# Kernel optimization log

Measured on AMD Instinct MI355X. Metric: run time of the kernel, lower is better.

The kernel has to match this reference:

```python
import jax, jax.numpy as jnp
import numpy as np

K = 8192   # codebook_size
D = 256    # latent_dim
COMMITMENT_COST = 0.25


def setup_inputs() -> dict:
    key = jax.random.key(0)
    kx, kw = jax.random.split(key)
    x = jax.random.normal(kx, (8, 4096, D), dtype=jnp.float32)
    # nn.init.uniform_(weight, -1/K, 1/K)
    weight = jax.random.uniform(kw, (K, D), dtype=jnp.float32,
                                minval=-1.0 / K, maxval=1.0 / K)
    return {"x": x, "weight": weight}


def reference(x, weight):
    sg = jax.lax.stop_gradient
    orig_shape = x.shape
    x_flat = x.reshape(-1, D)                      # [N, D]
    # squared euclidean distances; argmin identical to cdist argmin
    x_sq = jnp.sum(x_flat * x_flat, axis=-1, keepdims=True)      # [N, 1]
    w_sq = jnp.sum(weight * weight, axis=-1)                     # [K]
    dist2 = x_sq - 2.0 * (x_flat @ weight.T) + w_sq              # [N, K]
    indices = jnp.argmin(dist2, axis=1)                          # [N]
    quantized = jnp.take(weight, indices, axis=0).reshape(orig_shape)
    # eval / non-EMA branch of the torch module
    commitment_loss = jnp.mean((x - sg(quantized)) ** 2) * COMMITMENT_COST
    codebook_loss = jnp.mean((quantized - sg(x)) ** 2)
    total = commitment_loss + codebook_loss
    # straight-through estimator
    quantized_st = x + sg(quantized - x)
    indices_out = indices.reshape(orig_shape[:-1])
    return quantized_st, indices_out, commitment_loss, codebook_loss, total
```

## Files before the change

### kernel.cpp

```cpp
#include <hip/hip_runtime.h>

#define K_CB   8192
#define D_DIM  256
#define N_ROWS 32768
#define Q_ELEMS (N_ROWS * D_DIM)

#define M_FLAG 1.3e-4f
#define M_CAND 1.3e-4f
#define CAP    16

typedef __bf16 bf16x8 __attribute__((ext_vector_type(8)));
typedef float  f32x16 __attribute__((ext_vector_type(16)));

#define ASYNC_COPY16(gp, lp)                                              \
    __builtin_amdgcn_global_load_lds(                                     \
        (const __attribute__((address_space(1))) unsigned int*)(gp),      \
        (__attribute__((address_space(3))) unsigned int*)(lp), 16, 0, 0)


__device__ inline ushort f2bf(float f) {
    unsigned u = __float_as_uint(f);
    unsigned r = u + 0x7FFFu + ((u >> 16) & 1u);
    return (ushort)(r >> 16);
}

__device__ inline uint4 pack8(float4 a, float4 b) {
    uint4 o;
    o.x = (unsigned)f2bf(a.x) | ((unsigned)f2bf(a.y) << 16);
    o.y = (unsigned)f2bf(a.z) | ((unsigned)f2bf(a.w) << 16);
    o.z = (unsigned)f2bf(b.x) | ((unsigned)f2bf(b.y) << 16);
    o.w = (unsigned)f2bf(b.z) | ((unsigned)f2bf(b.w) << 16);
    return o;
}

__global__ __launch_bounds__(256) void wsq_wbf_kernel(const float* __restrict__ w,
                                                      float* __restrict__ wsq,
                                                      ushort* __restrict__ wbf) {
    __shared__ __align__(16) ushort tile[64 * 256];
    const int t = threadIdx.x;
    const int kb = blockIdx.x;
    const int wv = t >> 6, lane = t & 63;

    const float4* wb = reinterpret_cast<const float4*>(w) + (size_t)kb * 4096;
    #pragma unroll
    for (int i = 0; i < 16; ++i) {
        int j = i * 256 + t;
        float4 v = wb[j];
        int c = j >> 6, d4 = j & 63;
        uint2 o;
        o.x = (unsigned)f2bf(-2.0f * v.x) | ((unsigned)f2bf(-2.0f * v.y) << 16);
        o.y = (unsigned)f2bf(-2.0f * v.z) | ((unsigned)f2bf(-2.0f * v.w) << 16);
        *reinterpret_cast<uint2*>((char*)tile + (size_t)(d4 >> 1) * 1024 + c * 16 + (d4 & 1) * 8) = o;
    }

    for (int c = wv; c < 64; c += 4) {
        float4 v = reinterpret_cast<const float4*>(w)[(size_t)(kb * 64 + c) * 64 + lane];
        double sq = (double)v.x * v.x + (double)v.y * v.y + (double)v.z * v.z + (double)v.w * v.w;
        #pragma unroll
        for (int off = 32; off > 0; off >>= 1) sq += __shfl_down(sq, off, 64);
        if (lane == 0) wsq[kb * 64 + c] = (float)sq;
    }

    __syncthreads();
    const uint4* src = reinterpret_cast<const uint4*>(tile);
    uint4* dst = reinterpret_cast<uint4*>((char*)wbf + (size_t)kb * 32768);
    #pragma unroll
    for (int j = 0; j < 8; ++j) dst[j * 256 + t] = src[j * 256 + t];
}

__global__ __launch_bounds__(512, 2) void pass1_kernel(
        const float* __restrict__ x, const ushort* __restrict__ wbf,
        const float* __restrict__ wsq, float* __restrict__ idx_out,
        float* __restrict__ rowmin, int* __restrict__ flags,
        unsigned* __restrict__ flag_count, int* __restrict__ hard_flags,
        unsigned* __restrict__ hard_count, int* __restrict__ candcnt,
        int* __restrict__ cands) {
    __shared__ __align__(16) char smem[66560];
    ushort* wt = reinterpret_cast<ushort*>(smem);

    const int t = threadIdx.x;
    const int lane = t & 63, ln31 = lane & 31, h = lane >> 5;
    const int wv = t >> 6;
    const int rs = wv >> 1, cs = wv & 1;
    const int colL = cs * 32 + ln31;
    const int r0 = blockIdx.x * 128;

    {
        const char* g = (const char*)wbf + (size_t)wv * 4096 + (size_t)lane * 16;
        char* l = (char*)wt + wv * 4096;
        #pragma unroll
        for (int i = 0; i < 4; ++i) ASYNC_COPY16(g + i * 1024, l + i * 1024);
    }

    const int arow = r0 + rs * 32 + ln31;
    const float4* xr = reinterpret_cast<const float4*>(x) + (size_t)arow * 64;
    bf16x8 afr[16];
    #pragma unroll
    for (int kk = 0; kk < 16; ++kk)
        afr[kk] = __builtin_bit_cast(bf16x8, pack8(xr[kk * 4 + h * 2], xr[kk * 4 + h * 2 + 1]));

    float b1[16], b2[16];
    #pragma unroll
    for (int r = 0; r < 16; ++r) { b1[r] = 3.4e38f; b2[r] = 3.4e38f; }

    __syncthreads();

    int cur = 0;
    for (int it = 0; it < 128; ++it) {
        float wsk = wsq[it * 64 + colL];
        {
            const char* g = (const char*)wbf + (size_t)((it + 1) & 127) * 32768
                          + (size_t)wv * 4096 + (size_t)lane * 16;
            char* l = (char*)wt + (cur ^ 1) * 32768 + wv * 4096;
            #pragma unroll
            for (int i = 0; i < 4; ++i) ASYNC_COPY16(g + i * 1024, l + i * 1024);
        }

        const ushort* bt = wt + cur * 16384;
        f32x16 acc = {0,0,0,0,0,0,0,0,0,0,0,0,0,0,0,0};
        #pragma unroll
        for (int kk = 0; kk < 16; ++kk) {
            bf16x8 bf = *reinterpret_cast<const bf16x8*>(&bt[(size_t)(kk * 2 + h) * 512 + colL * 8]);
            acc = __builtin_amdgcn_mfma_f32_32x32x16_bf16(afr[kk], bf, acc, 0, 0, 0);
        }

        const int kb = it * 64 + colL;
        #pragma unroll
        for (int r = 0; r < 16; ++r) {
            float s0 = acc[r] + wsk;
            float p0 = __uint_as_float((__float_as_uint(s0) & 0xFFFFE000u) | (unsigned)kb);
            b2[r] = __builtin_amdgcn_fmed3f(p0, b1[r], b2[r]);
            b1[r] = fminf(p0, b1[r]);
        }

        __syncthreads();
        cur ^= 1;
    }

    float* sb1 = reinterpret_cast<float*>(smem);
    float* sb2 = sb1 + 128 * 65;
    #pragma unroll
    for (int r = 0; r < 16; ++r) {
        int rl = rs * 32 + (r & 3) + 8 * (r >> 2) + 4 * h;
        sb1[rl * 65 + colL] = b1[r];
        sb2[rl * 65 + colL] = b2[r];
    }
    __syncthreads();
    if (t < 128) {
        float B1 = 3.4e38f, B2 = 3.4e38f;
        for (int c = 0; c < 64; ++c) {
            float a1 = sb1[t * 65 + c], a2 = sb2[t * 65 + c];
            float nb2 = fminf(fmaxf(B1, a1), fminf(B2, a2));
            B1 = fminf(B1, a1);
            B2 = nb2;
        }
        int row = r0 + t;
        idx_out[row] = (float)(__float_as_uint(B1) & 0x1FFFu);
        rowmin[row]  = B1;
        int nc = 0;
        if (B2 - B1 <= M_FLAG) {
            unsigned pos = atomicAdd(flag_count, 1u);
            if (pos < N_ROWS) flags[pos] = row;
            float T = B1 + M_CAND;
            bool hard = false;
            for (int c = 0; c < 64; ++c) {
                float a1 = sb1[t * 65 + c];
                if (a1 <= T) {
                    if (nc < CAP) cands[row * CAP + nc] = (int)(__float_as_uint(a1) & 0x1FFFu);
                    ++nc;
                }
                if (sb2[t * 65 + c] <= T) hard = true;
            }
            if (nc > CAP) hard = true;
            if (hard) {
                nc = 0;
                unsigned hp = atomicAdd(hard_count, 1u);
                if (hp < N_ROWS) hard_flags[hp] = row;
            }
        }
        candcnt[row] = nc;
    }
}

__global__ __launch_bounds__(256, 2) void fixup_kernel(
        const float* __restrict__ x, const ushort* __restrict__ wbf,
        const float* __restrict__ wsq, const float* __restrict__ rowmin,
        const int* __restrict__ hard_flags, const unsigned* __restrict__ hard_count,
        int* __restrict__ candcnt, int* __restrict__ cands) {
    __shared__ __align__(16) ushort wt[64 * 256];
    __shared__ int   sh_rows[64];
    __shared__ float sh_thr[64];

    const int t = threadIdx.x;
    const int lane = t & 63, ln31 = lane & 31, h = lane >> 5;
    const int wv = t >> 6, rs = wv & 1, cs = wv >> 1;
    const int colL = cs * 32 + ln31;

    unsigned cu = hard_count[0];
    int cnt = cu > N_ROWS ? N_ROWS : (int)cu;
    int nunits = ((cnt + 63) >> 6) * 8;

    for (int u = blockIdx.x; u < nunits; u += 512) {
        int ksp  = u & 7;
        int base = (u >> 3) * 64;
        int nrows = cnt - base; if (nrows > 64) nrows = 64;

        __syncthreads();
        if (t < 64) {
            int valid = (t < nrows);
            int gr = hard_flags[base + (valid ? t : 0)];
            sh_rows[t] = gr;
            sh_thr[t]  = valid ? rowmin[gr] + M_CAND : -3.4e38f;
        }
        __syncthreads();

        int arow = sh_rows[rs * 32 + ln31];
        const float4* xr = reinterpret_cast<const float4*>(x) + (size_t)arow * 64;
        bf16x8 afr[16];
        #pragma unroll
        for (int kk = 0; kk < 16; ++kk)
            afr[kk] = __builtin_bit_cast(bf16x8, pack8(xr[kk * 4 + h * 2], xr[kk * 4 + h * 2 + 1]));
        float thr_r[16];
        int   rl_r[16];
        #pragma unroll
        for (int r = 0; r < 16; ++r) {
            rl_r[r]  = rs * 32 + (r & 3) + 8 * (r >> 2) + 4 * h;
            thr_r[r] = sh_thr[rl_r[r]];
        }

        for (int tb = 0; tb < 16; ++tb) {
            int blk = ksp * 16 + tb;
            __syncthreads();
            {
                const char* g = (const char*)wbf + (size_t)blk * 32768
                              + (size_t)wv * 8192 + (size_t)lane * 16;
                char* l = (char*)wt + wv * 8192;
                #pragma unroll
                for (int i = 0; i < 8; ++i) ASYNC_COPY16(g + i * 1024, l + i * 1024);
            }
            __syncthreads();

            int kcol = blk * 64 + colL;
            float wsk = wsq[kcol];
            f32x16 acc = {0,0,0,0,0,0,0,0,0,0,0,0,0,0,0,0};
            #pragma unroll
            for (int kk = 0; kk < 16; ++kk) {
                bf16x8 bf = *reinterpret_cast<const bf16x8*>(&wt[(size_t)(kk * 2 + h) * 512 + colL * 8]);
                acc = __builtin_amdgcn_mfma_f32_32x32x16_bf16(afr[kk], bf, acc, 0, 0, 0);
            }
            #pragma unroll
            for (int r = 0; r < 16; ++r) {
                float s0 = acc[r] + wsk;
                if (s0 <= thr_r[r]) {
                    int grow = sh_rows[rl_r[r]];
                    int pos = atomicAdd(&candcnt[grow], 1);
                    if (pos < CAP) cands[grow * CAP + pos] = kcol;
                }
            }
        }
    }
}

__global__ __launch_bounds__(256) void rescore_kernel(
        const float* __restrict__ x, const float* __restrict__ w,
        const float* __restrict__ wsq,
        const int* __restrict__ flags, const unsigned* __restrict__ flag_count,
        const int* __restrict__ candcnt, const int* __restrict__ cands,
        float* __restrict__ idx_out) {
    int wid  = (blockIdx.x * 256 + threadIdx.x) >> 6;
    int lane = threadIdx.x & 63;
    unsigned cu = flag_count[0];
    int cnt = (cu > N_ROWS) ? N_ROWS : (int)cu;

    for (int fi = wid; fi < cnt; fi += 1024) {
        int row = flags[fi];
        float4 xv = reinterpret_cast<const float4*>(x)[(size_t)row * 64 + lane];
        double xs = (double)xv.x * xv.x + (double)xv.y * xv.y
                  + (double)xv.z * xv.z + (double)xv.w * xv.w;
        #pragma unroll
        for (int off = 1; off < 64; off <<= 1) xs += __shfl_xor(xs, off, 64);
        float Xs = (float)xs;
        int nc = candcnt[row]; if (nc > CAP) nc = CAP;
        float bq = 3.4e38f; int bk = -1;
        for (int c = 0; c < nc; ++c) {
            int k = cands[row * CAP + c];
            float4 wv = reinterpret_cast<const float4*>(w)[(size_t)k * 64 + lane];
            double d = (double)xv.x * wv.x + (double)xv.y * wv.y
                     + (double)xv.z * wv.z + (double)xv.w * wv.w;
            #pragma unroll
            for (int off = 1; off < 64; off <<= 1) d += __shfl_xor(d, off, 64);
            float XW = (float)d;
            float t3 = fmaf(-2.0f, XW, Xs);
            float qv = t3 + wsq[k];
            if (qv < bq || (qv == bq && k < bk) || bk < 0) { bq = qv; bk = k; }
        }
        if (lane == 0 && bk >= 0) idx_out[row] = (float)bk;
    }
}

__global__ __launch_bounds__(256) void gather_loss_kernel(
        const float* __restrict__ x, const float* __restrict__ w,
        const float* __restrict__ idx_f, float* __restrict__ out_q,
        float* __restrict__ accum) {
    const int nf4 = Q_ELEMS / 4;
    float lsum = 0.0f;
    for (int e = blockIdx.x * blockDim.x + threadIdx.x; e < nf4;
         e += gridDim.x * blockDim.x) {
        int row = e >> 6, d4 = e & 63;
        int k = (int)idx_f[row];
        float4 xv = reinterpret_cast<const float4*>(x)[e];
        float4 qv = reinterpret_cast<const float4*>(w)[(size_t)k * 64 + d4];
        float4 ov;
        ov.x = xv.x + (qv.x - xv.x);
        ov.y = xv.y + (qv.y - xv.y);
        ov.z = xv.z + (qv.z - xv.z);
        ov.w = xv.w + (qv.w - xv.w);
        reinterpret_cast<float4*>(out_q)[e] = ov;
        float dx = xv.x - qv.x, dy = xv.y - qv.y, dz = xv.z - qv.z, dw = xv.w - qv.w;
        lsum += dx * dx + dy * dy + dz * dz + dw * dw;
    }
    #pragma unroll
    for (int off = 32; off > 0; off >>= 1) lsum += __shfl_down(lsum, off, 64);
    __shared__ float ssum[4];
    if ((threadIdx.x & 63) == 0) ssum[threadIdx.x >> 6] = lsum;
    __syncthreads();
    if (threadIdx.x == 0)
        atomicAdd(accum, ssum[0] + ssum[1] + ssum[2] + ssum[3]);
}

__global__ void finalize_kernel(const float* __restrict__ accum,
                                float* __restrict__ out_tail) {
    float mse = accum[0] / (float)Q_ELEMS;
    float commit = 0.25f * mse;
    out_tail[0] = commit;
    out_tail[1] = mse;
    out_tail[2] = commit + mse;
}

extern "C" void kernel_launch(void* const* d_in, const int* in_sizes, int n_in,
                              void* d_out, int out_size, void* d_ws, size_t ws_size,
                              hipStream_t stream) {
    const float* x = (const float*)d_in[0];
    const float* w = (const float*)d_in[1];
    float* out = (float*)d_out;

    char* ws = (char*)d_ws;
    float*    Wsq        = (float*)ws;
    float*    Rmin       = (float*)(ws + 163840);
    float*    accum      = (float*)(ws + 294912);
    unsigned* flag_count = (unsigned*)(ws + 294916);
    unsigned* hard_count = (unsigned*)(ws + 294920);
    int*      flags      = (int*)(ws + 294924);
    int*      hard_flags = (int*)(ws + 425996);
    int*      candcnt    = (int*)(ws + 557068);
    int*      cands      = (int*)(ws + 688140);
    ushort*   Wbf        = (ushort*)(ws + 2785296);

    hipMemsetAsync(ws + 294912, 0, 12, stream);
    wsq_wbf_kernel<<<K_CB / 64, 256, 0, stream>>>(w, Wsq, Wbf);
    pass1_kernel<<<N_ROWS / 128, 512, 0, stream>>>(x, Wbf, Wsq, out + Q_ELEMS,
                                                   Rmin, flags, flag_count,
                                                   hard_flags, hard_count,
                                                   candcnt, cands);
    fixup_kernel<<<512, 256, 0, stream>>>(x, Wbf, Wsq, Rmin, hard_flags, hard_count,
                                          candcnt, cands);
    rescore_kernel<<<256, 256, 0, stream>>>(x, w, Wsq, flags, flag_count,
                                            candcnt, cands, out + Q_ELEMS);
    gather_loss_kernel<<<8192, 256, 0, stream>>>(x, w, out + Q_ELEMS, out, accum);
    finalize_kernel<<<1, 1, 0, stream>>>(accum, out + Q_ELEMS + N_ROWS);
}
```

Baseline: 408.5 us.

## Deepen codebook LDS pipeline to four stages with single barrier per iteration

Replaces the double-buffered codebook tile pipeline in pass1 with a 4-slot ring that prefetches three tiles ahead. The per-tile squared norms are now staged into LDS alongside the weights. Each iteration uses explicit vmcnt waits plus a single barrier instead of a trailing __syncthreads, and raises wave priority around the MFMA loop. The aim is to hide global-load latency and cut barrier stalls, but LDS grows to about 135KB per block, which likely drops occupancy from two blocks per CU to one despite launch_bounds(512,2).

```diff
diff --git a/kernel.cpp b/kernel.cpp
--- a/kernel.cpp
+++ b/kernel.cpp
@@ -75,8 +75,7 @@
         unsigned* __restrict__ flag_count, int* __restrict__ hard_flags,
         unsigned* __restrict__ hard_count, int* __restrict__ candcnt,
         int* __restrict__ cands) {
-    __shared__ __align__(16) char smem[66560];
-    ushort* wt = reinterpret_cast<ushort*>(smem);
+    __shared__ __align__(16) char smem[135168];
 
     const int t = threadIdx.x;
     const int lane = t & 63, ln31 = lane & 31, h = lane >> 5;
@@ -85,11 +84,16 @@
     const int colL = cs * 32 + ln31;
     const int r0 = blockIdx.x * 128;
 
-    {
-        const char* g = (const char*)wbf + (size_t)wv * 4096 + (size_t)lane * 16;
-        char* l = (char*)wt + wv * 4096;
+    const char* gWb = (const char*)wbf + (size_t)wv * 4096 + (size_t)lane * 16;
+    const char* gQb = (const char*)wsq + (size_t)lane * 16;
+
+    #pragma unroll
+    for (int p = 0; p < 3; ++p) {
+        const char* g = gWb + (size_t)p * 32768;
+        char* l = smem + p * 33792 + wv * 4096;
         #pragma unroll
         for (int i = 0; i < 4; ++i) ASYNC_COPY16(g + i * 1024, l + i * 1024);
+        if (wv == 0) ASYNC_COPY16(gQb + p * 256, smem + p * 33792 + 32768);
     }
 
     const int arow = r0 + rs * 32 + ln31;
@@ -103,26 +107,33 @@
     #pragma unroll
     for (int r = 0; r < 16; ++r) { b1[r] = 3.4e38f; b2[r] = 3.4e38f; }
 
-    __syncthreads();
-
-    int cur = 0;
     for (int it = 0; it < 128; ++it) {
-        float wsk = wsq[it * 64 + colL];
+        if (wv == 0) { asm volatile("s_waitcnt vmcnt(10)" ::: "memory"); }
+        else         { asm volatile("s_waitcnt vmcnt(8)"  ::: "memory"); }
+        __builtin_amdgcn_s_barrier();
+
         {
-            const char* g = (const char*)wbf + (size_t)((it + 1) & 127) * 32768
-                          + (size_t)wv * 4096 + (size_t)lane * 16;
-            char* l = (char*)wt + (cur ^ 1) * 32768 + wv * 4096;
+            const int nt = (it + 3) & 127;
+            const int nb = (it + 3) & 3;
+            const char* g = gWb + (size_t)nt * 32768;
+            char* l = smem + nb * 33792 + wv * 4096;
             #pragma unroll
             for (int i = 0; i < 4; ++i) ASYNC_COPY16(g + i * 1024, l + i * 1024);
-        }
-
-        const ushort* bt = wt + cur * 16384;
+            if (wv == 0) ASYNC_COPY16(gQb + (size_t)nt * 256, smem + nb * 33792 + 32768);
+        }
+
+        const int cur = it & 3;
+        const ushort* bt = reinterpret_cast<const ushort*>(smem + cur * 33792);
+        float wsk = *reinterpret_cast<const float*>(smem + cur * 33792 + 32768 + colL * 4);
+
         f32x16 acc = {0,0,0,0,0,0,0,0,0,0,0,0,0,0,0,0};
+        __builtin_amdgcn_s_setprio(1);
         #pragma unroll
         for (int kk = 0; kk < 16; ++kk) {
-            bf16x8 bf = *reinterpret_cast<const bf16x8*>(&bt[(size_t)(kk * 2 + h) * 512 + colL * 8]);
+            bf16x8 bf = *reinterpret_cast<const bf16x8*>(&bt[(kk * 2 + h) * 512 + colL * 8]);
             acc = __builtin_amdgcn_mfma_f32_32x32x16_bf16(afr[kk], bf, acc, 0, 0, 0);
         }
+        __builtin_amdgcn_s_setprio(0);
 
         const int kb = it * 64 + colL;
         #pragma unroll
@@ -132,10 +143,9 @@
             b2[r] = __builtin_amdgcn_fmed3f(p0, b1[r], b2[r]);
             b1[r] = fminf(p0, b1[r]);
         }
-
-        __syncthreads();
-        cur ^= 1;
-    }
+    }
+
+    __syncthreads();
 
     float* sb1 = reinterpret_cast<float*>(smem);
     float* sb2 = sb1 + 128 * 65;
```

Measured after the change: 416.1 us. Within noise of the previous version (+1.9%).

## Retile pass1 to 64x32 per wave with 128-column codebook tiles

Applied to the files above, without the earlier changes.

Each wave now computes two 32-row MFMA tiles that share one B fragment, so every LDS load of codebook data feeds two MFMAs. The codebook tile per iteration grows to 128 columns, giving 64 iterations, and the weight-norm vector is staged once into LDS with async copies instead of being read from global memory each iteration. The loop switches to explicit s_barrier and vmcnt waits, and raises wave priority around the MFMA block. The cost is a much larger LDS allocation (160KB), which limits blocks per CU, and roughly double the register use for A fragments and running minima, which puts occupancy at risk.

```diff
diff --git a/kernel.cpp b/kernel.cpp
--- a/kernel.cpp
+++ b/kernel.cpp
@@ -75,81 +75,104 @@
         unsigned* __restrict__ flag_count, int* __restrict__ hard_flags,
         unsigned* __restrict__ hard_count, int* __restrict__ candcnt,
         int* __restrict__ cands) {
-    __shared__ __align__(16) char smem[66560];
-    ushort* wt = reinterpret_cast<ushort*>(smem);
+    __shared__ __align__(16) char smem[163840];
 
     const int t = threadIdx.x;
     const int lane = t & 63, ln31 = lane & 31, h = lane >> 5;
     const int wv = t >> 6;
-    const int rs = wv >> 1, cs = wv & 1;
-    const int colL = cs * 32 + ln31;
+    const int rg = wv >> 2;
+    const int cg = wv & 3;
+    const int colL = cg * 32 + ln31;
     const int r0 = blockIdx.x * 128;
 
+    const char* gWb = (const char*)wbf + (size_t)wv * 8192 + (size_t)lane * 16;
+
+    const int arow0 = r0 + rg * 64 + ln31;
+    const float4* xr0 = reinterpret_cast<const float4*>(x) + (size_t)arow0 * 64;
+    const float4* xr1 = xr0 + (size_t)32 * 64;
+    bf16x8 afr0[16], afr1[16];
+    #pragma unroll
+    for (int kk = 0; kk < 16; ++kk) {
+        afr0[kk] = __builtin_bit_cast(bf16x8, pack8(xr0[kk * 4 + h * 2], xr0[kk * 4 + h * 2 + 1]));
+        afr1[kk] = __builtin_bit_cast(bf16x8, pack8(xr1[kk * 4 + h * 2], xr1[kk * 4 + h * 2 + 1]));
+    }
+
     {
-        const char* g = (const char*)wbf + (size_t)wv * 4096 + (size_t)lane * 16;
-        char* l = (char*)wt + wv * 4096;
-        #pragma unroll
-        for (int i = 0; i < 4; ++i) ASYNC_COPY16(g + i * 1024, l + i * 1024);
-    }
-
-    const int arow = r0 + rs * 32 + ln31;
-    const float4* xr = reinterpret_cast<const float4*>(x) + (size_t)arow * 64;
-    bf16x8 afr[16];
-    #pragma unroll
-    for (int kk = 0; kk < 16; ++kk)
-        afr[kk] = __builtin_bit_cast(bf16x8, pack8(xr[kk * 4 + h * 2], xr[kk * 4 + h * 2 + 1]));
-
-    float b1[16], b2[16];
-    #pragma unroll
-    for (int r = 0; r < 16; ++r) { b1[r] = 3.4e38f; b2[r] = 3.4e38f; }
+        const char* gq = (const char*)wsq + (size_t)wv * 4096 + (size_t)lane * 16;
+        char* lq = smem + 131072 + wv * 4096;
+        #pragma unroll
+        for (int i = 0; i < 4; ++i) ASYNC_COPY16(gq + i * 1024, lq + i * 1024);
+        char* l0 = smem + wv * 8192;
+        #pragma unroll
+        for (int i = 0; i < 8; ++i) ASYNC_COPY16(gWb + i * 1024, l0 + i * 1024);
+    }
+
+    float b1a[16], b2a[16], b1b[16], b2b[16];
+    #pragma unroll
+    for (int r = 0; r < 16; ++r) { b1a[r] = 3.4e38f; b2a[r] = 3.4e38f;
+                                   b1b[r] = 3.4e38f; b2b[r] = 3.4e38f; }
+
+    const int rbase = (colL >> 6) * 16384 + (colL & 63) * 8;
+
+    for (int it = 0; it < 64; ++it) {
+        __builtin_amdgcn_s_barrier();
+        __builtin_amdgcn_sched_barrier(0);
+        {
+            const int nt = (it + 1) & 63;
+            const char* g = gWb + (size_t)nt * 65536;
+            char* l = smem + ((it + 1) & 1) * 65536 + wv * 8192;
+            #pragma unroll
+            for (int i = 0; i < 8; ++i) ASYNC_COPY16(g + i * 1024, l + i * 1024);
+        }
+        asm volatile("s_waitcnt vmcnt(8)" ::: "memory");
+        __builtin_amdgcn_s_barrier();
+        __builtin_amdgcn_sched_barrier(0);
+
+        const ushort* bt = reinterpret_cast<const ushort*>(smem + (it & 1) * 65536);
+        float wsk = *reinterpret_cast<const float*>(smem + 131072 + (size_t)(it * 128 + colL) * 4);
+
+        f32x16 acc0 = {0,0,0,0,0,0,0,0,0,0,0,0,0,0,0,0};
+        f32x16 acc1 = {0,0,0,0,0,0,0,0,0,0,0,0,0,0,0,0};
+        __builtin_amdgcn_s_setprio(1);
+        #pragma unroll
+        for (int kk = 0; kk < 16; ++kk) {
+            bf16x8 bf = *reinterpret_cast<const bf16x8*>(&bt[rbase + (kk * 2 + h) * 512]);
+            acc0 = __builtin_amdgcn_mfma_f32_32x32x16_bf16(afr0[kk], bf, acc0, 0, 0, 0);
+            acc1 = __builtin_amdgcn_mfma_f32_32x32x16_bf16(afr1[kk], bf, acc1, 0, 0, 0);
+        }
+        __builtin_amdgcn_s_setprio(0);
+
+        const int kb = it * 128 + colL;
+        #pragma unroll
+        for (int r = 0; r < 16; ++r) {
+            float s0 = acc0[r] + wsk;
+            float p0 = __uint_as_float((__float_as_uint(s0) & 0xFFFFE000u) | (unsigned)kb);
+            b2a[r] = __builtin_amdgcn_fmed3f(p0, b1a[r], b2a[r]);
+            b1a[r] = fminf(p0, b1a[r]);
+            float s1 = acc1[r] + wsk;
+            float p1 = __uint_as_float((__float_as_uint(s1) & 0xFFFFE000u) | (unsigned)kb);
+            b2b[r] = __builtin_amdgcn_fmed3f(p1, b1b[r], b2b[r]);
+            b1b[r] = fminf(p1, b1b[r]);
+        }
+    }
 
     __syncthreads();
 
-    int cur = 0;
-    for (int it = 0; it < 128; ++it) {
-        float wsk = wsq[it * 64 + colL];
-        {
-            const char* g = (const char*)wbf + (size_t)((it + 1) & 127) * 32768
-                          + (size_t)wv * 4096 + (size_t)lane * 16;
-            char* l = (char*)wt + (cur ^ 1) * 32768 + wv * 4096;
-            #pragma unroll
-            for (int i = 0; i < 4; ++i) ASYNC_COPY16(g + i * 1024, l + i * 1024);
-        }
-
-        const ushort* bt = wt + cur * 16384;
-        f32x16 acc = {0,0,0,0,0,0,0,0,0,0,0,0,0,0,0,0};
-        #pragma unroll
-        for (int kk = 0; kk < 16; ++kk) {
-            bf16x8 bf = *reinterpret_cast<const bf16x8*>(&bt[(size_t)(kk * 2 + h) * 512 + colL * 8]);
-            acc = __builtin_amdgcn_mfma_f32_32x32x16_bf16(afr[kk], bf, acc, 0, 0, 0);
-        }
-
-        const int kb = it * 64 + colL;
-        #pragma unroll
-        for (int r = 0; r < 16; ++r) {
-            float s0 = acc[r] + wsk;
-            float p0 = __uint_as_float((__float_as_uint(s0) & 0xFFFFE000u) | (unsigned)kb);
-            b2[r] = __builtin_amdgcn_fmed3f(p0, b1[r], b2[r]);
-            b1[r] = fminf(p0, b1[r]);
-        }
-
-        __syncthreads();
-        cur ^= 1;
-    }
-
     float* sb1 = reinterpret_cast<float*>(smem);
-    float* sb2 = sb1 + 128 * 65;
+    float* sb2 = sb1 + 128 * 129;
     #pragma unroll
     for (int r = 0; r < 16; ++r) {
-        int rl = rs * 32 + (r & 3) + 8 * (r >> 2) + 4 * h;
-        sb1[rl * 65 + colL] = b1[r];
-        sb2[rl * 65 + colL] = b2[r];
+        int rl = rg * 64 + (r & 3) + 8 * (r >> 2) + 4 * h;
+        sb1[rl * 129 + colL] = b1a[r];
+        sb2[rl * 129 + colL] = b2a[r];
+        sb1[(rl + 32) * 129 + colL] = b1b[r];
+        sb2[(rl + 32) * 129 + colL] = b2b[r];
     }
     __syncthreads();
     if (t < 128) {
         float B1 = 3.4e38f, B2 = 3.4e38f;
-        for (int c = 0; c < 64; ++c) {
-            float a1 = sb1[t * 65 + c], a2 = sb2[t * 65 + c];
+        for (int c = 0; c < 128; ++c) {
+            float a1 = sb1[t * 129 + c], a2 = sb2[t * 129 + c];
             float nb2 = fminf(fmaxf(B1, a1), fminf(B2, a2));
             B1 = fminf(B1, a1);
             B2 = nb2;
@@ -163,13 +186,13 @@
             if (pos < N_ROWS) flags[pos] = row;
             float T = B1 + M_CAND;
             bool hard = false;
-            for (int c = 0; c < 64; ++c) {
-                float a1 = sb1[t * 65 + c];
+            for (int c = 0; c < 128; ++c) {
+                float a1 = sb1[t * 129 + c];
                 if (a1 <= T) {
                     if (nc < CAP) cands[row * CAP + nc] = (int)(__float_as_uint(a1) & 0x1FFFu);
                     ++nc;
                 }
-                if (sb2[t * 65 + c] <= T) hard = true;
+                if (sb2[t * 129 + c] <= T) hard = true;
             }
             if (nc > CAP) hard = true;
             if (hard) {
```

Result: no change. 414.2 us (+1.4%).

## Retile pass1 to 64 rows x 128 codes per block with single-buffered LDS

Applied to the files above, without the earlier changes.

Pass1 now gives each block 64 rows and 128 codebook columns per step, so 8 waves cover 2 row groups by 4 column groups. The LDS tile is single-buffered with a barrier between the MFMA phase and the next async load, and MFMA issue is raised with setprio. This targets 4 blocks per CU for more overlap across blocks. The bf16 codebook layout is changed to 32-code sub-tiles, and fixup indexing is updated to match. The trade-off is less in-block prefetch, with latency hiding left to occupancy, plus twice as many blocks that each reload x.

```diff
diff --git a/kernel.cpp b/kernel.cpp
--- a/kernel.cpp
+++ b/kernel.cpp
@@ -50,7 +50,8 @@
         uint2 o;
         o.x = (unsigned)f2bf(-2.0f * v.x) | ((unsigned)f2bf(-2.0f * v.y) << 16);
         o.y = (unsigned)f2bf(-2.0f * v.z) | ((unsigned)f2bf(-2.0f * v.w) << 16);
-        *reinterpret_cast<uint2*>((char*)tile + (size_t)(d4 >> 1) * 1024 + c * 16 + (d4 & 1) * 8) = o;
+        *reinterpret_cast<uint2*>((char*)tile + (size_t)(c >> 5) * 16384
+                                  + (size_t)(d4 >> 1) * 512 + (c & 31) * 16 + (d4 & 1) * 8) = o;
     }
 
     for (int c = wv; c < 64; c += 4) {
@@ -68,31 +69,27 @@
     for (int j = 0; j < 8; ++j) dst[j * 256 + t] = src[j * 256 + t];
 }
 
-__global__ __launch_bounds__(512, 2) void pass1_kernel(
+__global__ __launch_bounds__(512, 4) void pass1_kernel(
         const float* __restrict__ x, const ushort* __restrict__ wbf,
         const float* __restrict__ wsq, float* __restrict__ idx_out,
         float* __restrict__ rowmin, int* __restrict__ flags,
         unsigned* __restrict__ flag_count, int* __restrict__ hard_flags,
         unsigned* __restrict__ hard_count, int* __restrict__ candcnt,
         int* __restrict__ cands) {
-    __shared__ __align__(16) char smem[66560];
-    ushort* wt = reinterpret_cast<ushort*>(smem);
+    __shared__ __align__(16) char smem[67584];
 
     const int t = threadIdx.x;
     const int lane = t & 63, ln31 = lane & 31, h = lane >> 5;
     const int wv = t >> 6;
-    const int rs = wv >> 1, cs = wv & 1;
-    const int colL = cs * 32 + ln31;
-    const int r0 = blockIdx.x * 128;
-
-    {
-        const char* g = (const char*)wbf + (size_t)wv * 4096 + (size_t)lane * 16;
-        char* l = (char*)wt + wv * 4096;
-        #pragma unroll
-        for (int i = 0; i < 4; ++i) ASYNC_COPY16(g + i * 1024, l + i * 1024);
-    }
-
-    const int arow = r0 + rs * 32 + ln31;
+    const int rg = wv >> 2;
+    const int cb = wv & 3;
+    const int kbL = cb * 32 + ln31;
+    const int r0 = blockIdx.x * 64;
+
+    const char* gW = (const char*)wbf + (size_t)wv * 8192 + (size_t)lane * 16;
+    char* lW = smem + wv * 8192;
+
+    const int arow = r0 + rg * 32 + ln31;
     const float4* xr = reinterpret_cast<const float4*>(x) + (size_t)arow * 64;
     bf16x8 afr[16];
     #pragma unroll
@@ -103,53 +100,58 @@
     #pragma unroll
     for (int r = 0; r < 16; ++r) { b1[r] = 3.4e38f; b2[r] = 3.4e38f; }
 
+    #pragma unroll
+    for (int i = 0; i < 8; ++i) ASYNC_COPY16(gW + i * 1024, lW + i * 1024);
+    float wskc = wsq[kbL];
     __syncthreads();
 
-    int cur = 0;
-    for (int it = 0; it < 128; ++it) {
-        float wsk = wsq[it * 64 + colL];
-        {
-            const char* g = (const char*)wbf + (size_t)((it + 1) & 127) * 32768
-                          + (size_t)wv * 4096 + (size_t)lane * 16;
-            char* l = (char*)wt + (cur ^ 1) * 32768 + wv * 4096;
+    for (int tt = 0; tt < 64; ++tt) {
+        f32x16 acc = {0,0,0,0,0,0,0,0,0,0,0,0,0,0,0,0};
+        __builtin_amdgcn_s_setprio(1);
+        #pragma unroll
+        for (int kk = 0; kk < 16; ++kk) {
+            bf16x8 bf = *reinterpret_cast<const bf16x8*>(
+                smem + cb * 16384 + (kk * 2 + h) * 512 + ln31 * 16);
+            acc = __builtin_amdgcn_mfma_f32_32x32x16_bf16(afr[kk], bf, acc, 0, 0, 0);
+        }
+        __builtin_amdgcn_s_setprio(0);
+
+        __syncthreads();
+
+        if (tt < 63) {
+            const char* gt = gW + (size_t)(tt + 1) * 65536;
             #pragma unroll
-            for (int i = 0; i < 4; ++i) ASYNC_COPY16(g + i * 1024, l + i * 1024);
-        }
-
-        const ushort* bt = wt + cur * 16384;
-        f32x16 acc = {0,0,0,0,0,0,0,0,0,0,0,0,0,0,0,0};
-        #pragma unroll
-        for (int kk = 0; kk < 16; ++kk) {
-            bf16x8 bf = *reinterpret_cast<const bf16x8*>(&bt[(size_t)(kk * 2 + h) * 512 + colL * 8]);
-            acc = __builtin_amdgcn_mfma_f32_32x32x16_bf16(afr[kk], bf, acc, 0, 0, 0);
-        }
-
-        const int kb = it * 64 + colL;
+            for (int i = 0; i < 8; ++i) ASYNC_COPY16(gt + i * 1024, lW + i * 1024);
+        }
+        float wskn = wsq[(size_t)(((tt + 1) & 63) * 128) + kbL];
+        __builtin_amdgcn_sched_barrier(0);
+
+        const int kb = tt * 128 + kbL;
         #pragma unroll
         for (int r = 0; r < 16; ++r) {
-            float s0 = acc[r] + wsk;
+            float s0 = acc[r] + wskc;
             float p0 = __uint_as_float((__float_as_uint(s0) & 0xFFFFE000u) | (unsigned)kb);
             b2[r] = __builtin_amdgcn_fmed3f(p0, b1[r], b2[r]);
             b1[r] = fminf(p0, b1[r]);
         }
+        wskc = wskn;
 
         __syncthreads();
-        cur ^= 1;
     }
 
     float* sb1 = reinterpret_cast<float*>(smem);
-    float* sb2 = sb1 + 128 * 65;
+    float* sb2 = sb1 + 64 * 129;
     #pragma unroll
     for (int r = 0; r < 16; ++r) {
-        int rl = rs * 32 + (r & 3) + 8 * (r >> 2) + 4 * h;
-        sb1[rl * 65 + colL] = b1[r];
-        sb2[rl * 65 + colL] = b2[r];
+        int rl = rg * 32 + (r & 3) + 8 * (r >> 2) + 4 * h;
+        sb1[rl * 129 + kbL] = b1[r];
+        sb2[rl * 129 + kbL] = b2[r];
     }
     __syncthreads();
-    if (t < 128) {
+    if (t < 64) {
         float B1 = 3.4e38f, B2 = 3.4e38f;
-        for (int c = 0; c < 64; ++c) {
-            float a1 = sb1[t * 65 + c], a2 = sb2[t * 65 + c];
+        for (int c = 0; c < 128; ++c) {
+            float a1 = sb1[t * 129 + c], a2 = sb2[t * 129 + c];
             float nb2 = fminf(fmaxf(B1, a1), fminf(B2, a2));
             B1 = fminf(B1, a1);
             B2 = nb2;
@@ -163,13 +165,13 @@
             if (pos < N_ROWS) flags[pos] = row;
             float T = B1 + M_CAND;
             bool hard = false;
-            for (int c = 0; c < 64; ++c) {
-                float a1 = sb1[t * 65 + c];
+            for (int c = 0; c < 128; ++c) {
+                float a1 = sb1[t * 129 + c];
                 if (a1 <= T) {
                     if (nc < CAP) cands[row * CAP + nc] = (int)(__float_as_uint(a1) & 0x1FFFu);
                     ++nc;
                 }
-                if (sb2[t * 65 + c] <= T) hard = true;
+                if (sb2[t * 129 + c] <= T) hard = true;
             }
             if (nc > CAP) hard = true;
             if (hard) {
@@ -245,7 +247,8 @@
             f32x16 acc = {0,0,0,0,0,0,0,0,0,0,0,0,0,0,0,0};
             #pragma unroll
             for (int kk = 0; kk < 16; ++kk) {
-                bf16x8 bf = *reinterpret_cast<const bf16x8*>(&wt[(size_t)(kk * 2 + h) * 512 + colL * 8]);
+                bf16x8 bf = *reinterpret_cast<const bf16x8*>(
+                    &wt[cs * 8192 + (kk * 2 + h) * 256 + ln31 * 8]);
                 acc = __builtin_amdgcn_mfma_f32_32x32x16_bf16(afr[kk], bf, acc, 0, 0, 0);
             }
             #pragma unroll
@@ -358,10 +361,10 @@
 
     hipMemsetAsync(ws + 294912, 0, 12, stream);
     wsq_wbf_kernel<<<K_CB / 64, 256, 0, stream>>>(w, Wsq, Wbf);
-    pass1_kernel<<<N_ROWS / 128, 512, 0, stream>>>(x, Wbf, Wsq, out + Q_ELEMS,
-                                                   Rmin, flags, flag_count,
-                                                   hard_flags, hard_count,
-                                                   candcnt, cands);
+    pass1_kernel<<<N_ROWS / 64, 512, 0, stream>>>(x, Wbf, Wsq, out + Q_ELEMS,
+                                                  Rmin, flags, flag_count,
+                                                  hard_flags, hard_count,
+                                                  candcnt, cands);
     fixup_kernel<<<512, 256, 0, stream>>>(x, Wbf, Wsq, Rmin, hard_flags, hard_count,
                                           candcnt, cands);
     rescore_kernel<<<256, 256, 0, stream>>>(x, w, Wsq, flags, flag_count,
```

New measurement: 430.8 us. 1.05x slower.
